# Performance work log

Measured on AMD Instinct MI355X. Metric: run time of the kernel, lower is better.

## Reference

```python
import jax, jax.numpy as jnp
import numpy as np

B, N, C, CS, CP, H, L = 1, 2048, 128, 128, 16, 4, 3
NQ, NK = 32, 128  # local attention window: n_queries, n_keys
EPS = 1e-5


def _make_beta(n):
    l = np.arange(n)[:, None]
    m = np.arange(n)[None, :]
    con = np.zeros((n, n), dtype=bool)
    for c in np.arange(NQ / 2, n, NQ):
        con |= (np.abs(l - c) < NQ / 2) & (np.abs(m - c) < NK / 2)
    return np.where(con, 0.0, -1e10).astype(np.float32)


def setup_inputs() -> dict:
    key = jax.random.key(0)
    ks = iter(jax.random.split(key, 32))
    w = lambda *shape: jax.random.normal(next(ks), shape, dtype=jnp.float32) * 0.02
    inp = {
        'a': jax.random.normal(next(ks), (B, N, C), dtype=jnp.float32),
        's': jax.random.normal(next(ks), (B, N, CS), dtype=jnp.float32),
        'z': jax.random.normal(next(ks), (B, N, N, CP), dtype=jnp.float32),
        'beta': jnp.asarray(_make_beta(N))[None],
        'ada1_ln_w': jnp.ones((L, CS)), 'ada1_lin_w': w(L, CS, C),
        'ada1_lin_b': jnp.zeros((L, C)), 'ada1_nb_w': w(L, CS, C),
        'lnz_w': jnp.ones((L, CP)), 'lnz_b': jnp.zeros((L, CP)),
        'zinj_w': w(L, CP, H),
        'q_w': w(L, C, C), 'q_b': jnp.zeros((L, C)),
        'k_w': w(L, C, C), 'v_w': w(L, C, C),
        'g_w': w(L, C, C), 'o_w': w(L, C, C),
        'agate_w': w(L, CS, C), 'agate_b': jnp.full((L, C), -2.0),
        'ada2_ln_w': jnp.ones((L, CS)), 'ada2_lin_w': w(L, CS, C),
        'ada2_lin_b': jnp.zeros((L, C)), 'ada2_nb_w': w(L, CS, C),
        'lin1_w': w(L, C, 2 * C), 'lin2_w': w(L, C, 2 * C), 'lin3_w': w(L, 2 * C, C),
        'tgate_w': w(L, CS, C), 'tgate_b': jnp.full((L, C), -2.0),
    }
    return inp


def _ln(x):
    mu = jnp.mean(x, axis=-1, keepdims=True)
    var = jnp.var(x, axis=-1, keepdims=True)
    return (x - mu) * jax.lax.rsqrt(var + EPS)


def _adaln(a, s, ln_w, lin_w, lin_b, nb_w):
    # AdaLN: LN(a) gated & shifted by LN(s)
    a = _ln(a)
    sn = _ln(s) * ln_w
    return jax.nn.sigmoid(sn @ lin_w + lin_b) * a + sn @ nb_w


def _forward(a, s, z, beta, ada1_ln_w, ada1_lin_w, ada1_lin_b, ada1_nb_w,
             lnz_w, lnz_b, zinj_w, q_w, q_b, k_w, v_w, g_w, o_w,
             agate_w, agate_b, ada2_ln_w, ada2_lin_w, ada2_lin_b, ada2_nb_w,
             lin1_w, lin2_w, lin3_w, tgate_w, tgate_b):
    b_, n_, c_ = a.shape
    h_ = zinj_w.shape[-1]
    d_ = c_ // h_
    scale = 1.0 / np.sqrt(d_).astype(np.float32)
    zn0 = _ln(z)  # shared pre-affine LN of pair rep
    for i in range(q_w.shape[0]):
        # --- AttentionPairBias ---
        ah = _adaln(a, s, ada1_ln_w[i], ada1_lin_w[i], ada1_lin_b[i], ada1_nb_w[i])
        zb = jnp.einsum('bijc,ch->bhij', zn0 * lnz_w[i] + lnz_b[i], zinj_w[i])
        q = ((ah @ q_w[i] + q_b[i]) * scale).reshape(b_, n_, h_, d_)
        k = (ah @ k_w[i]).reshape(b_, n_, h_, d_)
        v = (ah @ v_w[i]).reshape(b_, n_, h_, d_)
        scores = jnp.einsum('bihd,bjhd->bhij', q, k) + zb + beta[:, None]
        p = jax.nn.softmax(scores, axis=-1)
        o = jnp.einsum('bhij,bjhd->bihd', p, v).reshape(b_, n_, c_)
        o = o * jax.nn.sigmoid(ah @ g_w[i])
        attn = (o @ o_w[i]) * jax.nn.sigmoid(s @ agate_w[i] + agate_b[i])
        # --- ConditionedTransitionBlock ---
        th = _adaln(a, s, ada2_ln_w[i], ada2_lin_w[i], ada2_lin_b[i], ada2_nb_w[i])
        bb = jax.nn.silu(th @ lin1_w[i]) * (th @ lin2_w[i])
        trans = jax.nn.sigmoid(s @ tgate_w[i] + tgate_b[i]) * th * (bb @ lin3_w[i])
        a = attn + trans
    return a


def reference(a, s, z, beta, ada1_ln_w, ada1_lin_w, ada1_lin_b, ada1_nb_w,
              lnz_w, lnz_b, zinj_w, q_w, q_b, k_w, v_w, g_w, o_w,
              agate_w, agate_b, ada2_ln_w, ada2_lin_w, ada2_lin_b, ada2_nb_w,
              lin1_w, lin2_w, lin3_w, tgate_w, tgate_b):
    return _forward(a, s, z, beta, ada1_ln_w, ada1_lin_w, ada1_lin_b, ada1_nb_w,
                    lnz_w, lnz_b, zinj_w, q_w, q_b, k_w, v_w, g_w, o_w,
                    agate_w, agate_b, ada2_ln_w, ada2_lin_w, ada2_lin_b, ada2_nb_w,
                    lin1_w, lin2_w, lin3_w, tgate_w, tgate_b)
```

## Files before the change

kernel.cpp:

```cpp
#include <hip/hip_runtime.h>


#define NT 2048

__device__ __forceinline__ float sig_(float x) { return 1.0f / (1.0f + __expf(-x)); }

__device__ __forceinline__ float redsum32(float v) {
#pragma unroll
  for (int o = 16; o > 0; o >>= 1) v += __shfl_xor(v, o);
  return v;
}

__device__ __forceinline__ void mm4(const float* __restrict__ W, int ldw,
                                    const float* As_row, int K, int c0, float* acc) {
  const float* __restrict__ wp = W + c0;
  for (int k = 0; k < K; k += 4) {
    float4 a4 = *(const float4*)(As_row + k);
#pragma unroll
    for (int kk = 0; kk < 4; ++kk) {
      float a = ((const float*)&a4)[kk];
      float4 w0 = *(const float4*)(wp);
      acc[0] = fmaf(a, w0.x, acc[0]);
      acc[1] = fmaf(a, w0.y, acc[1]);
      acc[2] = fmaf(a, w0.z, acc[2]);
      acc[3] = fmaf(a, w0.w, acc[3]);
      wp += ldw;
    }
  }
}

__device__ __forceinline__ void mm4x2(const float* __restrict__ W1,
                                      const float* __restrict__ W2, int ldw,
                                      const float* As_row, int K, int c0,
                                      float* acc1, float* acc2) {
  const float* __restrict__ wp1 = W1 + c0;
  const float* __restrict__ wp2 = W2 + c0;
  for (int k = 0; k < K; k += 4) {
    float4 a4 = *(const float4*)(As_row + k);
#pragma unroll
    for (int kk = 0; kk < 4; ++kk) {
      float a = ((const float*)&a4)[kk];
      float4 w0 = *(const float4*)(wp1);
      float4 u0 = *(const float4*)(wp2);
      acc1[0] = fmaf(a, w0.x, acc1[0]);
      acc1[1] = fmaf(a, w0.y, acc1[1]);
      acc1[2] = fmaf(a, w0.z, acc1[2]);
      acc1[3] = fmaf(a, w0.w, acc1[3]);
      acc2[0] = fmaf(a, u0.x, acc2[0]);
      acc2[1] = fmaf(a, u0.y, acc2[1]);
      acc2[2] = fmaf(a, u0.z, acc2[2]);
      acc2[3] = fmaf(a, u0.w, acc2[3]);
      wp1 += ldw; wp2 += ldw;
    }
  }
}

__global__ __launch_bounds__(256) void k_ln_rows(const float* __restrict__ X,
                                                 float* __restrict__ Y) {
  int row  = blockIdx.x * 4 + (threadIdx.x >> 6);
  int lane = threadIdx.x & 63;
  const float* xr = X + (size_t)row * 128;
  float x0 = xr[lane], x1 = xr[lane + 64];
  float s = x0 + x1;
#pragma unroll
  for (int o = 32; o > 0; o >>= 1) s += __shfl_xor(s, o);
  float mu = s * (1.0f / 128.0f);
  float d0 = x0 - mu, d1 = x1 - mu;
  float v = d0 * d0 + d1 * d1;
#pragma unroll
  for (int o = 32; o > 0; o >>= 1) v += __shfl_xor(v, o);
  float rs = rsqrtf(v * (1.0f / 128.0f) + 1e-5f);
  float* yr = Y + (size_t)row * 128;
  yr[lane] = d0 * rs;
  yr[lane + 64] = d1 * rs;
}

__global__ __launch_bounds__(256) void k_gates(
    const float* __restrict__ s, const float* __restrict__ agw,
    const float* __restrict__ agb, const float* __restrict__ tgw,
    const float* __restrict__ tgb, float* __restrict__ gatesA,
    float* __restrict__ gatesT) {
  __shared__ float As[8 * 132];
  int r0 = blockIdx.x * 8;
  int bz = blockIdx.y;
  int l = bz % 3, which = bz / 3;
  const float* W = (which ? tgw : agw) + (size_t)l * 128 * 128;
  const float* bias = (which ? tgb : agb) + (size_t)l * 128;
  float* outp = (which ? gatesT : gatesA) + (size_t)l * NT * 128;
  int tid = threadIdx.x;
  int r = tid >> 5, sub = tid & 31;
  *(float4*)&As[r * 132 + sub * 4] =
      *(const float4*)(s + (size_t)(r0 + r) * 128 + sub * 4);
  __syncthreads();
  int c0 = sub << 2;
  float acc[4] = {0, 0, 0, 0};
  mm4(W, 128, &As[r * 132], 128, c0, acc);
  size_t base = (size_t)(r0 + r) * 128 + c0;
#pragma unroll
  for (int j = 0; j < 4; ++j) outp[base + j] = sig_(acc[j] + bias[c0 + j]);
}

__global__ __launch_bounds__(256) void k_adaln12(
    const float* __restrict__ a, const float* __restrict__ ln_s,
    const float* __restrict__ lnw1, const float* __restrict__ linw1,
    const float* __restrict__ linb1, const float* __restrict__ nbw1,
    const float* __restrict__ lnw2, const float* __restrict__ linw2,
    const float* __restrict__ linb2, const float* __restrict__ nbw2,
    float* __restrict__ ah, float* __restrict__ th) {
  __shared__ float Sn[8 * 132];
  __shared__ float La[8 * 132];
  int r0 = blockIdx.x * 8;
  int y = blockIdx.y;
  const float* lnw  = y ? lnw2 : lnw1;
  const float* linw = y ? linw2 : linw1;
  const float* linb = y ? linb2 : linb1;
  const float* nbw  = y ? nbw2 : nbw1;
  float* outp = y ? th : ah;
  int tid = threadIdx.x;
  int r = tid >> 5, sub = tid & 31;
  {
    float4 v = *(const float4*)(ln_s + (size_t)(r0 + r) * 128 + sub * 4);
    float4 sc = *(const float4*)(lnw + sub * 4);
    v.x *= sc.x; v.y *= sc.y; v.z *= sc.z; v.w *= sc.w;
    *(float4*)&Sn[r * 132 + sub * 4] = v;
  }
  {
    float4 x = *(const float4*)(a + (size_t)(r0 + r) * 128 + sub * 4);
    float s = redsum32(x.x + x.y + x.z + x.w);
    float mu = s * (1.0f / 128.0f);
    float4 d = make_float4(x.x - mu, x.y - mu, x.z - mu, x.w - mu);
    float v = redsum32(d.x * d.x + d.y * d.y + d.z * d.z + d.w * d.w);
    float rs = rsqrtf(v * (1.0f / 128.0f) + 1e-5f);
    d.x *= rs; d.y *= rs; d.z *= rs; d.w *= rs;
    *(float4*)&La[r * 132 + sub * 4] = d;
  }
  __syncthreads();
  int c0 = sub << 2;
  float acc1[4] = {0, 0, 0, 0}, acc2[4] = {0, 0, 0, 0};
  mm4x2(linw, nbw, 128, &Sn[r * 132], 128, c0, acc1, acc2);
  size_t base = (size_t)(r0 + r) * 128 + c0;
#pragma unroll
  for (int j = 0; j < 4; ++j) {
    float g = sig_(acc1[j] + linb[c0 + j]);
    outp[base + j] = g * La[r * 132 + c0 + j] + acc2[j];
  }
}

__global__ __launch_bounds__(256) void k_qkvg(
    const float* __restrict__ ah, const float* __restrict__ qw,
    const float* __restrict__ kw, const float* __restrict__ vw,
    const float* __restrict__ gw, const float* __restrict__ qb,
    float* __restrict__ qkvg) {
  __shared__ float As[8 * 132];
  int r0 = blockIdx.x * 8;
  int mat = blockIdx.y;
  const float* W = (mat == 0) ? qw : (mat == 1) ? kw : (mat == 2) ? vw : gw;
  int tid = threadIdx.x;
  int r = tid >> 5, sub = tid & 31;
  *(float4*)&As[r * 132 + sub * 4] =
      *(const float4*)(ah + (size_t)(r0 + r) * 128 + sub * 4);
  __syncthreads();
  int c0 = sub << 2;
  float acc[4] = {0, 0, 0, 0};
  mm4(W, 128, &As[r * 132], 128, c0, acc);
  float* op = qkvg + (size_t)(r0 + r) * 512 + mat * 128 + c0;
  if (mat == 0) {
#pragma unroll
    for (int j = 0; j < 4; ++j)
      op[j] = (acc[j] + qb[c0 + j]) * 0.17677669529663687f;
  } else if (mat == 3) {
#pragma unroll
    for (int j = 0; j < 4; ++j) op[j] = sig_(acc[j]);
  } else {
#pragma unroll
    for (int j = 0; j < 4; ++j) op[j] = acc[j];
  }
}

__global__ __launch_bounds__(256) void k_wattn(
    const float* __restrict__ qkvg, const float* __restrict__ z,
    const float* __restrict__ lnzw, const float* __restrict__ lnzb,
    const float* __restrict__ zinj, float* __restrict__ og,
    float* __restrict__ colpart) {
  __shared__ float Qs[8][128];
  __shared__ float S[8][4][132];
  __shared__ float KV[32][128];
  __shared__ float wz[4][16];
  __shared__ float bzw[2][4];
  __shared__ float red[2][128];

  const int tid = threadIdx.x;
  const int bx = blockIdx.x;
  if (bx >= 256) {
    int b = bx - 256;
    int rr = tid >> 7, c = tid & 127;
    float acc = 0.0f;
    for (int t = 0; t < 16; ++t) {
      int row = b * 32 + rr + t * 2;
      acc += qkvg[(size_t)row * 512 + 256 + c];
    }
    red[rr][c] = acc;
    __syncthreads();
    if (rr == 0) colpart[b * 128 + c] = red[0][c] + red[1][c];
    return;
  }

  const int win = bx >> 2, sub4 = bx & 3;
  const int cen = 16 + 32 * win;
  const int i0 = cen - 15 + 8 * sub4;
  const int nrows = (sub4 == 3) ? 7 : 8;
  const int jlo = max(0, cen - 63), jhi = min(2047, cen + 63);
  const int nk = jhi - jlo + 1;

  if (tid < 64) {
    int h = tid & 3, c = tid >> 2;
    wz[h][c] = lnzw[c] * zinj[c * 4 + h];
  }
  if (tid < 8) {
    int h = tid & 3, which = tid >> 2;
    float acc = 0.0f;
    for (int c = 0; c < 16; ++c) acc += (which ? lnzb[c] : lnzw[c]) * zinj[c * 4 + h];
    bzw[which][h] = acc;
  }
  {
    int r = tid >> 5, sub = tid & 31;
    int i = i0 + min(r, nrows - 1);
    *(float4*)&Qs[r][sub * 4] = *(const float4*)(qkvg + (size_t)i * 512 + sub * 4);
  }
  __syncthreads();

  for (int idx = tid; idx < 8 * 128; idx += 256) {
    int r = idx >> 7, jj = idx & 127;
    if (jj < nk) {
      int i = i0 + min(r, nrows - 1);
      int j = jlo + jj;
      const float* zp = z + ((size_t)i * 2048 + j) * 16;
      float x[16];
      *(float4*)&x[0]  = *(const float4*)(zp + 0);
      *(float4*)&x[4]  = *(const float4*)(zp + 4);
      *(float4*)&x[8]  = *(const float4*)(zp + 8);
      *(float4*)&x[12] = *(const float4*)(zp + 12);
      float sm = 0.0f;
#pragma unroll
      for (int c = 0; c < 16; ++c) sm += x[c];
      float mu = sm * (1.0f / 16.0f);
      float var = 0.0f;
#pragma unroll
      for (int c = 0; c < 16; ++c) { float d = x[c] - mu; var = fmaf(d, d, var); }
      float rs = rsqrtf(var * (1.0f / 16.0f) + 1e-5f);
#pragma unroll
      for (int h = 0; h < 4; ++h) {
        float dot = 0.0f;
#pragma unroll
        for (int c = 0; c < 16; ++c) dot = fmaf(x[c], wz[h][c], dot);
        S[r][h][jj] = fmaf(rs, dot - mu * bzw[0][h], bzw[1][h]);
      }
    } else {
#pragma unroll
      for (int h = 0; h < 4; ++h) S[r][h][jj] = -1e30f;
    }
  }
  __syncthreads();

  {
    const int r = tid >> 5, h = (tid >> 3) & 3, part = tid & 7;
    float qreg[32];
#pragma unroll
    for (int d4 = 0; d4 < 32; d4 += 4)
      *(float4*)&qreg[d4] = *(const float4*)&Qs[r][h * 32 + d4];
    for (int kb = 0; kb < 128; kb += 32) {
      for (int idx = tid; idx < 32 * 32; idx += 256) {
        int kk = idx >> 5, c4 = (idx & 31) << 2;
        int j = jlo + kb + kk;
        int cs = (c4 + ((kk >> 3) << 2)) & 127;
        float4 val = make_float4(0.f, 0.f, 0.f, 0.f);
        if (j <= jhi) val = *(const float4*)(qkvg + (size_t)j * 512 + 128 + c4);
        *(float4*)&KV[kk][cs] = val;
      }
      __syncthreads();
#pragma unroll
      for (int u = 0; u < 4; ++u) {
        int jj = part + (u << 3);
        int rot = (jj >> 3) << 2;
        float dot = 0.0f;
#pragma unroll
        for (int d4 = 0; d4 < 32; d4 += 4) {
          int cs = (h * 32 + d4 + rot) & 127;
          float4 kv = *(const float4*)&KV[jj][cs];
          dot = fmaf(qreg[d4 + 0], kv.x, dot);
          dot = fmaf(qreg[d4 + 1], kv.y, dot);
          dot = fmaf(qreg[d4 + 2], kv.z, dot);
          dot = fmaf(qreg[d4 + 3], kv.w, dot);
        }
        S[r][h][kb + jj] += dot;
      }
      __syncthreads();
    }
  }

  {
    const int rh = tid >> 3, part = tid & 7;
    const int sr = rh >> 2, sh = rh & 3;
    float* Srow = &S[sr][sh][0];
    float m = -1e30f;
#pragma unroll
    for (int st = 0; st < 16; ++st) m = fmaxf(m, Srow[part + (st << 3)]);
#pragma unroll
    for (int o = 4; o > 0; o >>= 1) m = fmaxf(m, __shfl_xor(m, o));
    float ss = 0.0f;
#pragma unroll
    for (int st = 0; st < 16; ++st) {
      int jj = part + (st << 3);
      float e = __expf(Srow[jj] - m);
      Srow[jj] = e;
      ss += e;
    }
#pragma unroll
    for (int o = 4; o > 0; o >>= 1) ss += __shfl_xor(ss, o);
    float inv = 1.0f / ss;
#pragma unroll
    for (int st = 0; st < 16; ++st) Srow[part + (st << 3)] *= inv;
  }
  __syncthreads();

  {
    const int r = tid >> 5, cg = tid & 31;
    const int ca = cg << 2;
    const int h = cg >> 3;
    float acc[4] = {0, 0, 0, 0};
    for (int kb = 0; kb < 128; kb += 32) {
      for (int idx = tid; idx < 32 * 32; idx += 256) {
        int kk = idx >> 5, c4 = (idx & 31) << 2;
        int j = jlo + kb + kk;
        int cs = (c4 + ((kk >> 3) << 2)) & 127;
        float4 val = make_float4(0.f, 0.f, 0.f, 0.f);
        if (j <= jhi) val = *(const float4*)(qkvg + (size_t)j * 512 + 256 + c4);
        *(float4*)&KV[kk][cs] = val;
      }
      __syncthreads();
#pragma unroll 4
      for (int kk = 0; kk < 32; ++kk) {
        int rot = (kk >> 3) << 2;
        float sa = S[r][h][kb + kk];
        float4 va = *(const float4*)&KV[kk][(ca + rot) & 127];
        acc[0] = fmaf(sa, va.x, acc[0]);
        acc[1] = fmaf(sa, va.y, acc[1]);
        acc[2] = fmaf(sa, va.z, acc[2]);
        acc[3] = fmaf(sa, va.w, acc[3]);
      }
      __syncthreads();
    }
    if (r < nrows) {
      int i = i0 + r;
      float4 ga = *(const float4*)(qkvg + (size_t)i * 512 + 384 + ca);
      float4 oa = make_float4(acc[0] * ga.x, acc[1] * ga.y, acc[2] * ga.z, acc[3] * ga.w);
      *(float4*)(og + (size_t)i * 128 + ca) = oa;
    }
  }
}

__global__ __launch_bounds__(256) void k_oproj(const float* __restrict__ og,
                                               const float* __restrict__ ow,
                                               const float* __restrict__ gA,
                                               const float* __restrict__ colpart,
                                               const float* __restrict__ qkvg,
                                               float* __restrict__ attn) {
  __shared__ float As[8 * 132];
  __shared__ float red[2][128];
  int r0 = blockIdx.x * 8;
  int tid = threadIdx.x;
  int r = tid >> 5, sub = tid & 31;
  *(float4*)&As[r * 132 + sub * 4] =
      *(const float4*)(og + (size_t)(r0 + r) * 128 + sub * 4);
  __syncthreads();
  if ((r0 & 31) == 0) {
    int col = tid & 127, half = tid >> 7;
    float acc = 0.0f;
    for (int b = half; b < 64; b += 2) acc += colpart[b * 128 + col];
    red[half][col] = acc;
    __syncthreads();
    if (half == 0) {
      float mv = (red[0][col] + red[1][col]) * (1.0f / 2048.0f);
      As[col] = mv * qkvg[(size_t)r0 * 512 + 384 + col];
    }
    __syncthreads();
  }
  int c0 = sub << 2;
  float acc[4] = {0, 0, 0, 0};
  mm4(ow, 128, &As[r * 132], 128, c0, acc);
  size_t base = (size_t)(r0 + r) * 128 + c0;
#pragma unroll
  for (int j = 0; j < 4; ++j) attn[base + j] = acc[j] * gA[base + j];
}

__global__ __launch_bounds__(256) void k_lin12(const float* __restrict__ th,
                                               const float* __restrict__ w1,
                                               const float* __restrict__ w2,
                                               float* __restrict__ bb) {
  __shared__ float As[8 * 132];
  int r0 = blockIdx.x * 8;
  int cb0 = blockIdx.y * 128;
  int tid = threadIdx.x;
  int r = tid >> 5, sub = tid & 31;
  *(float4*)&As[r * 132 + sub * 4] =
      *(const float4*)(th + (size_t)(r0 + r) * 128 + sub * 4);
  __syncthreads();
  int c0 = cb0 + (sub << 2);
  float acc1[4] = {0, 0, 0, 0}, acc2[4] = {0, 0, 0, 0};
  mm4x2(w1, w2, 256, &As[r * 132], 128, c0, acc1, acc2);
  size_t base = (size_t)(r0 + r) * 256 + c0;
#pragma unroll
  for (int j = 0; j < 4; ++j) {
    float x1 = acc1[j];
    bb[base + j] = x1 * sig_(x1) * acc2[j];
  }
}

__global__ __launch_bounds__(256) void k_lin3comb(
    const float* __restrict__ bb, const float* __restrict__ w3,
    const float* __restrict__ attn, const float* __restrict__ gT,
    const float* __restrict__ th, float* __restrict__ outp) {
  __shared__ float As[8 * 260];
  int r0 = blockIdx.x * 8;
  int tid = threadIdx.x;
  for (int idx = tid; idx < 8 * 64; idx += 256) {
    int row = idx >> 6, c4 = (idx & 63) << 2;
    *(float4*)&As[row * 260 + c4] = *(const float4*)(bb + (size_t)(r0 + row) * 256 + c4);
  }
  __syncthreads();
  int r = tid >> 5, sub = tid & 31;
  int c0 = sub << 2;
  float acc[4] = {0, 0, 0, 0};
  mm4(w3, 128, &As[r * 260], 256, c0, acc);
  size_t base = (size_t)(r0 + r) * 128 + c0;
#pragma unroll
  for (int j = 0; j < 4; ++j)
    outp[base + j] = attn[base + j] + gT[base + j] * th[base + j] * acc[j];
}

extern "C" void kernel_launch(void* const* d_in, const int* in_sizes, int n_in,
                              void* d_out, int out_size, void* d_ws, size_t ws_size,
                              hipStream_t stream) {
  (void)in_sizes; (void)n_in; (void)out_size; (void)ws_size;
  const float* A_in   = (const float*)d_in[0];
  const float* S_in   = (const float*)d_in[1];
  const float* Z_in   = (const float*)d_in[2];
  const float* ada1_ln_w  = (const float*)d_in[4];
  const float* ada1_lin_w = (const float*)d_in[5];
  const float* ada1_lin_b = (const float*)d_in[6];
  const float* ada1_nb_w  = (const float*)d_in[7];
  const float* lnz_w      = (const float*)d_in[8];
  const float* lnz_b      = (const float*)d_in[9];
  const float* zinj_w     = (const float*)d_in[10];
  const float* q_w        = (const float*)d_in[11];
  const float* q_b        = (const float*)d_in[12];
  const float* k_w        = (const float*)d_in[13];
  const float* v_w        = (const float*)d_in[14];
  const float* g_w        = (const float*)d_in[15];
  const float* o_w        = (const float*)d_in[16];
  const float* agate_w    = (const float*)d_in[17];
  const float* agate_b    = (const float*)d_in[18];
  const float* ada2_ln_w  = (const float*)d_in[19];
  const float* ada2_lin_w = (const float*)d_in[20];
  const float* ada2_lin_b = (const float*)d_in[21];
  const float* ada2_nb_w  = (const float*)d_in[22];
  const float* lin1_w     = (const float*)d_in[23];
  const float* lin2_w     = (const float*)d_in[24];
  const float* lin3_w     = (const float*)d_in[25];
  const float* tgate_w    = (const float*)d_in[26];
  const float* tgate_b    = (const float*)d_in[27];

  const int N = NT, C = 128;
  float* ws = (float*)d_ws;
  float* ln_s    = ws;
  float* ah      = ln_s + (size_t)N * C;
  float* th      = ah + (size_t)N * C;
  float* qkvg    = th + (size_t)N * C;
  float* og      = qkvg + (size_t)N * 512;
  float* attn    = og + (size_t)N * C;
  float* bb      = attn + (size_t)N * C;
  float* gatesA  = bb + (size_t)N * 256;
  float* gatesT  = gatesA + (size_t)3 * N * C;
  float* colpart = gatesT + (size_t)3 * N * C;

  dim3 blk(256);
  k_ln_rows<<<512, blk, 0, stream>>>(S_in, ln_s);
  k_gates<<<dim3(256, 6), blk, 0, stream>>>(S_in, agate_w, agate_b, tgate_w,
                                            tgate_b, gatesA, gatesT);
  const float* acur = A_in;
  for (int l = 0; l < 3; ++l) {
    k_adaln12<<<dim3(256, 2), blk, 0, stream>>>(
        acur, ln_s, ada1_ln_w + (size_t)l * C, ada1_lin_w + (size_t)l * C * C,
        ada1_lin_b + (size_t)l * C, ada1_nb_w + (size_t)l * C * C,
        ada2_ln_w + (size_t)l * C, ada2_lin_w + (size_t)l * C * C,
        ada2_lin_b + (size_t)l * C, ada2_nb_w + (size_t)l * C * C, ah, th);
    k_qkvg<<<dim3(256, 4), blk, 0, stream>>>(ah, q_w + (size_t)l * C * C,
                                             k_w + (size_t)l * C * C,
                                             v_w + (size_t)l * C * C,
                                             g_w + (size_t)l * C * C,
                                             q_b + (size_t)l * C, qkvg);
    k_lin12<<<dim3(256, 2), blk, 0, stream>>>(th, lin1_w + (size_t)l * C * 2 * C,
                                              lin2_w + (size_t)l * C * 2 * C, bb);
    k_wattn<<<320, blk, 0, stream>>>(qkvg, Z_in, lnz_w + (size_t)l * 16,
                                     lnz_b + (size_t)l * 16,
                                     zinj_w + (size_t)l * 64, og, colpart);
    k_oproj<<<256, blk, 0, stream>>>(og, o_w + (size_t)l * C * C,
                                     gatesA + (size_t)l * N * C, colpart, qkvg,
                                     attn);
    k_lin3comb<<<256, blk, 0, stream>>>(bb, lin3_w + (size_t)l * 2 * C * C, attn,
                                        gatesT + (size_t)l * N * C, th,
                                        (float*)d_out);
    acur = (const float*)d_out;
  }
}
```

Before: 778.9 us.

## Fuse AdaLN, QKVG and lin12 projections; fuse oproj, gates and lin3 epilogue

Merges the per-layer pipeline into two fused kernels around the attention kernel. The first computes the AdaLN rows and keeps them in shared memory to feed the QKVG or lin1/lin2 GEMMs. The second does the output projection, the attention and transition gate GEMMs, and lin3 in one pass. This cuts kernel launches and global round trips for ah, attn and the precomputed gates. In exchange, the gate GEMMs and the LayerNorm of s are recomputed every layer, and each block now does more serial GEMM work with fewer blocks in flight.

Result: slower. 993.1 us (+27.5%).

```diff
diff --git a/kernel.cpp b/kernel.cpp
--- a/kernel.cpp
+++ b/kernel.cpp
@@ -55,125 +55,89 @@
   }
 }
 
-__global__ __launch_bounds__(256) void k_ln_rows(const float* __restrict__ X,
-                                                 float* __restrict__ Y) {
-  int row  = blockIdx.x * 4 + (threadIdx.x >> 6);
-  int lane = threadIdx.x & 63;
-  const float* xr = X + (size_t)row * 128;
-  float x0 = xr[lane], x1 = xr[lane + 64];
-  float s = x0 + x1;
-#pragma unroll
-  for (int o = 32; o > 0; o >>= 1) s += __shfl_xor(s, o);
-  float mu = s * (1.0f / 128.0f);
-  float d0 = x0 - mu, d1 = x1 - mu;
-  float v = d0 * d0 + d1 * d1;
-#pragma unroll
-  for (int o = 32; o > 0; o >>= 1) v += __shfl_xor(v, o);
-  float rs = rsqrtf(v * (1.0f / 128.0f) + 1e-5f);
-  float* yr = Y + (size_t)row * 128;
-  yr[lane] = d0 * rs;
-  yr[lane + 64] = d1 * rs;
-}
-
-__global__ __launch_bounds__(256) void k_gates(
-    const float* __restrict__ s, const float* __restrict__ agw,
-    const float* __restrict__ agb, const float* __restrict__ tgw,
-    const float* __restrict__ tgb, float* __restrict__ gatesA,
-    float* __restrict__ gatesT) {
-  __shared__ float As[8 * 132];
-  int r0 = blockIdx.x * 8;
-  int bz = blockIdx.y;
-  int l = bz % 3, which = bz / 3;
-  const float* W = (which ? tgw : agw) + (size_t)l * 128 * 128;
-  const float* bias = (which ? tgb : agb) + (size_t)l * 128;
-  float* outp = (which ? gatesT : gatesA) + (size_t)l * NT * 128;
-  int tid = threadIdx.x;
-  int r = tid >> 5, sub = tid & 31;
-  *(float4*)&As[r * 132 + sub * 4] =
-      *(const float4*)(s + (size_t)(r0 + r) * 128 + sub * 4);
-  __syncthreads();
-  int c0 = sub << 2;
-  float acc[4] = {0, 0, 0, 0};
-  mm4(W, 128, &As[r * 132], 128, c0, acc);
-  size_t base = (size_t)(r0 + r) * 128 + c0;
-#pragma unroll
-  for (int j = 0; j < 4; ++j) outp[base + j] = sig_(acc[j] + bias[c0 + j]);
-}
-
-__global__ __launch_bounds__(256) void k_adaln12(
-    const float* __restrict__ a, const float* __restrict__ ln_s,
+__global__ __launch_bounds__(256) void k_fused1(
+    const float* __restrict__ a, const float* __restrict__ s,
     const float* __restrict__ lnw1, const float* __restrict__ linw1,
     const float* __restrict__ linb1, const float* __restrict__ nbw1,
+    const float* __restrict__ qw, const float* __restrict__ kw,
+    const float* __restrict__ vw, const float* __restrict__ gw,
+    const float* __restrict__ qb,
     const float* __restrict__ lnw2, const float* __restrict__ linw2,
     const float* __restrict__ linb2, const float* __restrict__ nbw2,
-    float* __restrict__ ah, float* __restrict__ th) {
+    const float* __restrict__ w1, const float* __restrict__ w2,
+    float* __restrict__ th, float* __restrict__ qkvg, float* __restrict__ bb) {
   __shared__ float Sn[8 * 132];
   __shared__ float La[8 * 132];
-  int r0 = blockIdx.x * 8;
-  int y = blockIdx.y;
+  __shared__ float Hh[8 * 132];
+  const int r0 = blockIdx.x * 8;
+  const int y = blockIdx.y;
   const float* lnw  = y ? lnw2 : lnw1;
   const float* linw = y ? linw2 : linw1;
   const float* linb = y ? linb2 : linb1;
   const float* nbw  = y ? nbw2 : nbw1;
-  float* outp = y ? th : ah;
-  int tid = threadIdx.x;
-  int r = tid >> 5, sub = tid & 31;
-  {
-    float4 v = *(const float4*)(ln_s + (size_t)(r0 + r) * 128 + sub * 4);
-    float4 sc = *(const float4*)(lnw + sub * 4);
-    v.x *= sc.x; v.y *= sc.y; v.z *= sc.z; v.w *= sc.w;
-    *(float4*)&Sn[r * 132 + sub * 4] = v;
-  }
-  {
-    float4 x = *(const float4*)(a + (size_t)(r0 + r) * 128 + sub * 4);
-    float s = redsum32(x.x + x.y + x.z + x.w);
-    float mu = s * (1.0f / 128.0f);
+  const int tid = threadIdx.x;
+  const int r = tid >> 5, sub = tid & 31, c0 = sub << 2;
+  {
+    float4 x = *(const float4*)(s + (size_t)(r0 + r) * 128 + c0);
+    float sm = redsum32(x.x + x.y + x.z + x.w);
+    float mu = sm * (1.0f / 128.0f);
+    float4 d = make_float4(x.x - mu, x.y - mu, x.z - mu, x.w - mu);
+    float v = redsum32(d.x * d.x + d.y * d.y + d.z * d.z + d.w * d.w);
+    float rs = rsqrtf(v * (1.0f / 128.0f) + 1e-5f);
+    float4 sc = *(const float4*)(lnw + c0);
+    d.x *= rs * sc.x; d.y *= rs * sc.y; d.z *= rs * sc.z; d.w *= rs * sc.w;
+    *(float4*)&Sn[r * 132 + c0] = d;
+  }
+  {
+    float4 x = *(const float4*)(a + (size_t)(r0 + r) * 128 + c0);
+    float sm = redsum32(x.x + x.y + x.z + x.w);
+    float mu = sm * (1.0f / 128.0f);
     float4 d = make_float4(x.x - mu, x.y - mu, x.z - mu, x.w - mu);
     float v = redsum32(d.x * d.x + d.y * d.y + d.z * d.z + d.w * d.w);
     float rs = rsqrtf(v * (1.0f / 128.0f) + 1e-5f);
     d.x *= rs; d.y *= rs; d.z *= rs; d.w *= rs;
-    *(float4*)&La[r * 132 + sub * 4] = d;
-  }
-  __syncthreads();
-  int c0 = sub << 2;
-  float acc1[4] = {0, 0, 0, 0}, acc2[4] = {0, 0, 0, 0};
-  mm4x2(linw, nbw, 128, &Sn[r * 132], 128, c0, acc1, acc2);
-  size_t base = (size_t)(r0 + r) * 128 + c0;
-#pragma unroll
-  for (int j = 0; j < 4; ++j) {
-    float g = sig_(acc1[j] + linb[c0 + j]);
-    outp[base + j] = g * La[r * 132 + c0 + j] + acc2[j];
-  }
-}
-
-__global__ __launch_bounds__(256) void k_qkvg(
-    const float* __restrict__ ah, const float* __restrict__ qw,
-    const float* __restrict__ kw, const float* __restrict__ vw,
-    const float* __restrict__ gw, const float* __restrict__ qb,
-    float* __restrict__ qkvg) {
-  __shared__ float As[8 * 132];
-  int r0 = blockIdx.x * 8;
-  int mat = blockIdx.y;
-  const float* W = (mat == 0) ? qw : (mat == 1) ? kw : (mat == 2) ? vw : gw;
-  int tid = threadIdx.x;
-  int r = tid >> 5, sub = tid & 31;
-  *(float4*)&As[r * 132 + sub * 4] =
-      *(const float4*)(ah + (size_t)(r0 + r) * 128 + sub * 4);
-  __syncthreads();
-  int c0 = sub << 2;
-  float acc[4] = {0, 0, 0, 0};
-  mm4(W, 128, &As[r * 132], 128, c0, acc);
-  float* op = qkvg + (size_t)(r0 + r) * 512 + mat * 128 + c0;
-  if (mat == 0) {
-#pragma unroll
-    for (int j = 0; j < 4; ++j)
-      op[j] = (acc[j] + qb[c0 + j]) * 0.17677669529663687f;
-  } else if (mat == 3) {
-#pragma unroll
-    for (int j = 0; j < 4; ++j) op[j] = sig_(acc[j]);
+    *(float4*)&La[r * 132 + c0] = d;
+  }
+  __syncthreads();
+  {
+    float acc1[4] = {0, 0, 0, 0}, acc2[4] = {0, 0, 0, 0};
+    mm4x2(linw, nbw, 128, &Sn[r * 132], 128, c0, acc1, acc2);
+#pragma unroll
+    for (int j = 0; j < 4; ++j) {
+      float g = sig_(acc1[j] + linb[c0 + j]);
+      Hh[r * 132 + c0 + j] = g * La[r * 132 + c0 + j] + acc2[j];
+    }
+    if (y == 1) {
+      size_t base = (size_t)(r0 + r) * 128 + c0;
+#pragma unroll
+      for (int j = 0; j < 4; ++j) th[base + j] = Hh[r * 132 + c0 + j];
+    }
+  }
+  __syncthreads();
+  if (y == 0) {
+    float aq[4] = {0, 0, 0, 0}, ak[4] = {0, 0, 0, 0};
+    float av[4] = {0, 0, 0, 0}, ag[4] = {0, 0, 0, 0};
+    mm4x2(qw, kw, 128, &Hh[r * 132], 128, c0, aq, ak);
+    mm4x2(vw, gw, 128, &Hh[r * 132], 128, c0, av, ag);
+    float* op = qkvg + (size_t)(r0 + r) * 512;
+#pragma unroll
+    for (int j = 0; j < 4; ++j) {
+      op[c0 + j]       = (aq[j] + qb[c0 + j]) * 0.17677669529663687f;
+      op[128 + c0 + j] = ak[j];
+      op[256 + c0 + j] = av[j];
+      op[384 + c0 + j] = sig_(ag[j]);
+    }
   } else {
-#pragma unroll
-    for (int j = 0; j < 4; ++j) op[j] = acc[j];
+    float a1[4] = {0, 0, 0, 0}, a2[4] = {0, 0, 0, 0};
+    mm4x2(w1, w2, 256, &Hh[r * 132], 128, c0, a1, a2);
+    float b1[4] = {0, 0, 0, 0}, b2[4] = {0, 0, 0, 0};
+    mm4x2(w1, w2, 256, &Hh[r * 132], 128, c0 + 128, b1, b2);
+    size_t base = (size_t)(r0 + r) * 256;
+#pragma unroll
+    for (int j = 0; j < 4; ++j) {
+      bb[base + c0 + j]       = a1[j] * sig_(a1[j]) * a2[j];
+      bb[base + 128 + c0 + j] = b1[j] * sig_(b1[j]) * b2[j];
+    }
   }
 }
 
@@ -359,19 +323,27 @@
   }
 }
 
-__global__ __launch_bounds__(256) void k_oproj(const float* __restrict__ og,
-                                               const float* __restrict__ ow,
-                                               const float* __restrict__ gA,
-                                               const float* __restrict__ colpart,
-                                               const float* __restrict__ qkvg,
-                                               float* __restrict__ attn) {
-  __shared__ float As[8 * 132];
+__global__ __launch_bounds__(256) void k_fused2(
+    const float* __restrict__ og, const float* __restrict__ qkvg,
+    const float* __restrict__ colpart, const float* __restrict__ s,
+    const float* __restrict__ th, const float* __restrict__ bb,
+    const float* __restrict__ ow, const float* __restrict__ agw,
+    const float* __restrict__ agb, const float* __restrict__ tgw,
+    const float* __restrict__ tgb, const float* __restrict__ w3,
+    float* __restrict__ outp) {
+  __shared__ float Og[8 * 132];
+  __shared__ float Ss[8 * 132];
+  __shared__ float Bb[8 * 260];
   __shared__ float red[2][128];
-  int r0 = blockIdx.x * 8;
-  int tid = threadIdx.x;
-  int r = tid >> 5, sub = tid & 31;
-  *(float4*)&As[r * 132 + sub * 4] =
-      *(const float4*)(og + (size_t)(r0 + r) * 128 + sub * 4);
+  const int r0 = blockIdx.x * 8;
+  const int tid = threadIdx.x;
+  const int r = tid >> 5, sub = tid & 31, c0 = sub << 2;
+  *(float4*)&Og[r * 132 + c0] = *(const float4*)(og + (size_t)(r0 + r) * 128 + c0);
+  *(float4*)&Ss[r * 132 + c0] = *(const float4*)(s + (size_t)(r0 + r) * 128 + c0);
+  for (int idx = tid; idx < 8 * 64; idx += 256) {
+    int row = idx >> 6, cc = (idx & 63) << 2;
+    *(float4*)&Bb[row * 260 + cc] = *(const float4*)(bb + (size_t)(r0 + row) * 256 + cc);
+  }
   __syncthreads();
   if ((r0 & 31) == 0) {
     int col = tid & 127, half = tid >> 7;
@@ -381,61 +353,24 @@
     __syncthreads();
     if (half == 0) {
       float mv = (red[0][col] + red[1][col]) * (1.0f / 2048.0f);
-      As[col] = mv * qkvg[(size_t)r0 * 512 + 384 + col];
+      Og[col] = mv * qkvg[(size_t)r0 * 512 + 384 + col];
     }
     __syncthreads();
   }
-  int c0 = sub << 2;
-  float acc[4] = {0, 0, 0, 0};
-  mm4(ow, 128, &As[r * 132], 128, c0, acc);
+  float aO[4] = {0, 0, 0, 0}, aA[4] = {0, 0, 0, 0};
+  float aT[4] = {0, 0, 0, 0}, a3[4] = {0, 0, 0, 0};
+  mm4(ow, 128, &Og[r * 132], 128, c0, aO);
+  mm4x2(agw, tgw, 128, &Ss[r * 132], 128, c0, aA, aT);
+  mm4(w3, 128, &Bb[r * 260], 256, c0, a3);
   size_t base = (size_t)(r0 + r) * 128 + c0;
-#pragma unroll
-  for (int j = 0; j < 4; ++j) attn[base + j] = acc[j] * gA[base + j];
-}
-
-__global__ __launch_bounds__(256) void k_lin12(const float* __restrict__ th,
-                                               const float* __restrict__ w1,
-                                               const float* __restrict__ w2,
-                                               float* __restrict__ bb) {
-  __shared__ float As[8 * 132];
-  int r0 = blockIdx.x * 8;
-  int cb0 = blockIdx.y * 128;
-  int tid = threadIdx.x;
-  int r = tid >> 5, sub = tid & 31;
-  *(float4*)&As[r * 132 + sub * 4] =
-      *(const float4*)(th + (size_t)(r0 + r) * 128 + sub * 4);
-  __syncthreads();
-  int c0 = cb0 + (sub << 2);
-  float acc1[4] = {0, 0, 0, 0}, acc2[4] = {0, 0, 0, 0};
-  mm4x2(w1, w2, 256, &As[r * 132], 128, c0, acc1, acc2);
-  size_t base = (size_t)(r0 + r) * 256 + c0;
+  float4 thv = *(const float4*)(th + base);
+  const float* tp = (const float*)&thv;
 #pragma unroll
   for (int j = 0; j < 4; ++j) {
-    float x1 = acc1[j];
-    bb[base + j] = x1 * sig_(x1) * acc2[j];
-  }
-}
-
-__global__ __launch_bounds__(256) void k_lin3comb(
-    const float* __restrict__ bb, const float* __restrict__ w3,
-    const float* __restrict__ attn, const float* __restrict__ gT,
-    const float* __restrict__ th, float* __restrict__ outp) {
-  __shared__ float As[8 * 260];
-  int r0 = blockIdx.x * 8;
-  int tid = threadIdx.x;
-  for (int idx = tid; idx < 8 * 64; idx += 256) {
-    int row = idx >> 6, c4 = (idx & 63) << 2;
-    *(float4*)&As[row * 260 + c4] = *(const float4*)(bb + (size_t)(r0 + row) * 256 + c4);
-  }
-  __syncthreads();
-  int r = tid >> 5, sub = tid & 31;
-  int c0 = sub << 2;
-  float acc[4] = {0, 0, 0, 0};
-  mm4(w3, 128, &As[r * 260], 256, c0, acc);
-  size_t base = (size_t)(r0 + r) * 128 + c0;
-#pragma unroll
-  for (int j = 0; j < 4; ++j)
-    outp[base + j] = attn[base + j] + gT[base + j] * th[base + j] * acc[j];
+    float attn = aO[j] * sig_(aA[j] + agb[c0 + j]);
+    float trans = sig_(aT[j] + tgb[c0 + j]) * tp[j] * a3[j];
+    outp[base + j] = attn + trans;
+  }
 }
 
 extern "C" void kernel_launch(void* const* d_in, const int* in_sizes, int n_in,
@@ -472,44 +407,37 @@
 
   const int N = NT, C = 128;
   float* ws = (float*)d_ws;
-  float* ln_s    = ws;
-  float* ah      = ln_s + (size_t)N * C;
-  float* th      = ah + (size_t)N * C;
+  float* th      = ws;
   float* qkvg    = th + (size_t)N * C;
   float* og      = qkvg + (size_t)N * 512;
-  float* attn    = og + (size_t)N * C;
-  float* bb      = attn + (size_t)N * C;
-  float* gatesA  = bb + (size_t)N * 256;
-  float* gatesT  = gatesA + (size_t)3 * N * C;
-  float* colpart = gatesT + (size_t)3 * N * C;
+  float* bb      = og + (size_t)N * C;
+  float* colpart = bb + (size_t)N * 256;
 
   dim3 blk(256);
-  k_ln_rows<<<512, blk, 0, stream>>>(S_in, ln_s);
-  k_gates<<<dim3(256, 6), blk, 0, stream>>>(S_in, agate_w, agate_b, tgate_w,
-                                            tgate_b, gatesA, gatesT);
   const float* acur = A_in;
   for (int l = 0; l < 3; ++l) {
-    k_adaln12<<<dim3(256, 2), blk, 0, stream>>>(
-        acur, ln_s, ada1_ln_w + (size_t)l * C, ada1_lin_w + (size_t)l * C * C,
+    k_fused1<<<dim3(256, 2), blk, 0, stream>>>(
+        acur, S_in,
+        ada1_ln_w + (size_t)l * C, ada1_lin_w + (size_t)l * C * C,
         ada1_lin_b + (size_t)l * C, ada1_nb_w + (size_t)l * C * C,
+        q_w + (size_t)l * C * C, k_w + (size_t)l * C * C,
+        v_w + (size_t)l * C * C, g_w + (size_t)l * C * C,
+        q_b + (size_t)l * C,
         ada2_ln_w + (size_t)l * C, ada2_lin_w + (size_t)l * C * C,
-        ada2_lin_b + (size_t)l * C, ada2_nb_w + (size_t)l * C * C, ah, th);
-    k_qkvg<<<dim3(256, 4), blk, 0, stream>>>(ah, q_w + (size_t)l * C * C,
-                                             k_w + (size_t)l * C * C,
-                                             v_w + (size_t)l * C * C,
-                                             g_w + (size_t)l * C * C,
-                                             q_b + (size_t)l * C, qkvg);
-    k_lin12<<<dim3(256, 2), blk, 0, stream>>>(th, lin1_w + (size_t)l * C * 2 * C,
-                                              lin2_w + (size_t)l * C * 2 * C, bb);
+        ada2_lin_b + (size_t)l * C, ada2_nb_w + (size_t)l * C * C,
+        lin1_w + (size_t)l * C * 2 * C, lin2_w + (size_t)l * C * 2 * C,
+        th, qkvg, bb);
     k_wattn<<<320, blk, 0, stream>>>(qkvg, Z_in, lnz_w + (size_t)l * 16,
                                      lnz_b + (size_t)l * 16,
                                      zinj_w + (size_t)l * 64, og, colpart);
-    k_oproj<<<256, blk, 0, stream>>>(og, o_w + (size_t)l * C * C,
-                                     gatesA + (size_t)l * N * C, colpart, qkvg,
-                                     attn);
-    k_lin3comb<<<256, blk, 0, stream>>>(bb, lin3_w + (size_t)l * 2 * C * C, attn,
-                                        gatesT + (size_t)l * N * C, th,
-                                        (float*)d_out);
+    k_fused2<<<256, blk, 0, stream>>>(og, qkvg, colpart, S_in, th, bb,
+                                      o_w + (size_t)l * C * C,
+                                      agate_w + (size_t)l * C * C,
+                                      agate_b + (size_t)l * C,
+                                      tgate_w + (size_t)l * C * C,
+                                      tgate_b + (size_t)l * C,
+                                      lin3_w + (size_t)l * 2 * C * C,
+                                      (float*)d_out);
     acur = (const float*)d_out;
   }
 }
```
